# Optimization experiments

Measured on AMD Instinct MI355X. Metric: run time of the kernel, lower is better.

Reference implementation:

```python
import jax, jax.numpy as jnp
import numpy as np

B, H, S, DK, DV = 4, 16, 2048, 64, 64

def setup_inputs() -> dict:
    key = jax.random.key(0)
    k1, k2, k3, k4 = jax.random.split(key, 4)
    Q = jax.random.normal(k1, (B, H, S, DK), dtype=jnp.float32)
    K = jax.random.normal(k2, (B, H, S, DK), dtype=jnp.float32)
    V = jax.random.normal(k3, (B, H, S, DV), dtype=jnp.float32)
    mask_out = jax.random.randint(k4, (B, 1, 1, S), 0, 2).astype(jnp.bool_)
    return {"Q": Q, "K": K, "V": V, "mask_out": mask_out}

def reference(Q, K, V, mask_out):
    key_size = Q.shape[-1]
    seq_q, seq_k = Q.shape[-2], K.shape[-2]
    scale = jnp.sqrt(jnp.float32(key_size))
    # scores: [B, H, Sq, Sk]
    scores = jnp.einsum('bhqd,bhkd->bhqk', Q, K) / scale
    scores = jnp.where(mask_out, jnp.float32(-1e9), scores)
    attn = jax.nn.softmax(scores, axis=-1)
    # Gaussian relative-position decay: exp(-|i-j|^2 / (Sk^2 / 2))
    idx_q = jnp.arange(seq_q, dtype=jnp.float32)[:, None]
    idx_k = jnp.arange(seq_k, dtype=jnp.float32)[None, :]
    rel = idx_q - idx_k  # [Sq, Sk]
    decay = jnp.exp(-(rel * rel) * (2.0 / (seq_k * seq_k)))  # [Sq, Sk]
    attn = attn * decay  # broadcast over [B, H]
    return jnp.einsum('bhqk,bhkv->bhqv', attn, V)
```

## Files before the change

kernel.cpp:

```cpp
#include <hip/hip_runtime.h>
#include <hip/hip_bf16.h>
#include <hip/hip_fp16.h>

typedef __attribute__((ext_vector_type(8))) short bf16x8;
typedef __attribute__((ext_vector_type(4))) short bf16x4;
typedef __attribute__((ext_vector_type(4))) float f32x4;
typedef __attribute__((ext_vector_type(4))) unsigned u32x4;
typedef __attribute__((ext_vector_type(4))) int i32x4;

constexpr int Bn = 4, Hn = 16, S = 2048, D = 64;
constexpr int BQ = 128;
constexpr float LOG2E = 1.44269504088896340736f;
constexpr float CD2f = (2.0f / ((float)S * (float)S)) * LOG2E;

__device__ __forceinline__ unsigned cvtpk(float lo, float hi) {
    unsigned r;
    asm("v_cvt_pk_bf16_f32 %0, %1, %2" : "=v"(r) : "v"(lo), "v"(hi));
    return r;
}

__device__ __forceinline__ f32x4 mfma16(bf16x4 a, bf16x4 b, f32x4 c) {
#if __has_builtin(__builtin_amdgcn_mfma_f32_16x16x16bf16_1k)
    return __builtin_amdgcn_mfma_f32_16x16x16bf16_1k(a, b, c, 0, 0, 0);
#else
    asm volatile("v_mfma_f32_16x16x16_bf16 %0, %1, %2, %0"
                 : "+v"(c) : "v"(a), "v"(b));
    return c;
#endif
}

__device__ __forceinline__ void gload16(const short* g, short* lds) {
    __builtin_amdgcn_global_load_lds(
        (const __attribute__((address_space(1))) unsigned*)g,
        (__attribute__((address_space(3))) unsigned*)lds,
        16, 0, 0);
}

__global__ void compact_mask(const void* __restrict__ maskg,
                             int* __restrict__ idxp, int* __restrict__ Mg) {
    const int b = blockIdx.x, t = threadIdx.x;
    __shared__ int wsum[4];
    __shared__ int Msh;

    const unsigned* mu = (const unsigned*)maskg;
    bool is_bytes = false;
    #pragma unroll 8
    for (int i = 0; i < 64; ++i) is_bytes |= (mu[i] > 1u);

    int keep[8]; int cnt = 0;
    #pragma unroll
    for (int i = 0; i < 8; ++i) {
        const int key = t * 8 + i;
        int m;
        if (is_bytes) m = ((const unsigned char*)maskg)[b * S + key];
        else          m = ((const int*)maskg)[b * S + key];
        keep[i] = (m == 0);
        cnt += keep[i];
    }
    const int l = t & 63, w = t >> 6;
    int pre = cnt;
    #pragma unroll
    for (int d = 1; d < 64; d <<= 1) {
        int v = __shfl_up(pre, d, 64);
        if (l >= d) pre += v;
    }
    if (l == 63) wsum[w] = pre;
    __syncthreads();
    int base = 0;
    for (int i = 0; i < w; ++i) base += wsum[i];
    int offs = base + pre - cnt;
    #pragma unroll
    for (int i = 0; i < 8; ++i)
        if (keep[i]) idxp[b * S + (offs++)] = t * 8 + i;
    if (t == 255) Msh = base + pre;
    __syncthreads();
    const int M = Msh;
    for (int i = M + t; i < S; i += 256) idxp[b * S + i] = 0;
    if (M == 0)
        for (int i = t; i < S; i += 256) idxp[b * S + i] = i;
    if (t == 0) Mg[b] = (M == 0) ? -1 : M;
}

__global__ void pack_kv(const float* __restrict__ Kg, const float* __restrict__ Vg,
                        const int* __restrict__ idxp, const int* __restrict__ Mg,
                        short* __restrict__ Kw, short* __restrict__ Vw) {
    const int bh = blockIdx.x, b = bh >> 4;
    const int ck0 = blockIdx.y * 256;
    const int t = threadIdx.x;
    const int Mraw = Mg[b];
    const int M = (Mraw < 0) ? S : Mraw;
    if (ck0 >= M) return;
    const int* idxb = idxp + b * S;
    const float* Kp = Kg + (size_t)bh * S * D;
    const float* Vp = Vg + (size_t)bh * S * D;

    {
        const int dc = (t & 7) * 8;
        #pragma unroll
        for (int tile = 0; tile < 4; ++tile)
            #pragma unroll
            for (int it = 0; it < 2; ++it) {
                const int key = ck0 + tile * 64 + (t >> 3) + it * 32;
                u32x4 pk = u32x4{0u, 0u, 0u, 0u};
                if (key < M) {
                    const float* src = Kp + (size_t)idxb[key] * D + dc;
                    #pragma unroll
                    for (int jj = 0; jj < 4; ++jj)
                        pk[jj] = cvtpk(src[2 * jj], src[2 * jj + 1]);
                }
                *(u32x4*)(Kw + ((size_t)bh * S + key) * D + dc) = pk;
            }
    }
    {
        const int dv = t & 63;
        const int kb = (t >> 6) * 16;
        #pragma unroll
        for (int tile = 0; tile < 4; ++tile) {
            const int tg = (ck0 >> 6) + tile;
            float f[16];
            #pragma unroll
            for (int i = 0; i < 16; ++i) {
                const int key = ck0 + tile * 64 + kb + i;
                float v = 0.f;
                if (key < M) {
                    int row = idxb[key];
                    row = __builtin_amdgcn_readfirstlane(row);
                    v = Vp[(size_t)row * D + dv];
                }
                f[i] = v;
            }
            u32x4 p0, p1;
            #pragma unroll
            for (int jj = 0; jj < 4; ++jj) {
                p0[jj] = cvtpk(f[2 * jj], f[2 * jj + 1]);
                p1[jj] = cvtpk(f[8 + 2 * jj], f[9 + 2 * jj]);
            }
            short* dst = Vw + (((size_t)bh * 32 + tg) * 64 + dv) * 64 + kb;
            *(u32x4*)dst = p0;
            *(u32x4*)(dst + 8) = p1;
        }
    }
}

__global__ __launch_bounds__(256, 4) void attn_packed(
    const float* __restrict__ Qg, const short* __restrict__ Kw,
    const short* __restrict__ Vw, const int* __restrict__ idxp,
    const int* __restrict__ Mg, float* __restrict__ outg)
{
    __shared__ alignas(16) short Kt[2][64][64];
    __shared__ alignas(16) short Vt[2][64][64];
    __shared__ alignas(16) __half dtab[2176];
    __shared__ alignas(16) int   idxs[2][64];

    const int bid  = blockIdx.x;
    const int lblk = ((bid & 7) << 7) | (bid >> 3);
    const int qt   = lblk & 15;
    const int bh   = lblk >> 4;
    const int b    = bh >> 4;
    const int q0   = qt * BQ;

    const float* Qp   = Qg + ((size_t)bh * S + q0) * D;
    const short* Ksrc = Kw + (size_t)bh * S * D;
    const short* Vsrc = Vw + (size_t)bh * 32 * 64 * 64;
    float*       Op   = outg + ((size_t)bh * S + q0) * D;
    const int*   idxb = idxp + b * S;

    const int t  = threadIdx.x;
    const int w  = t >> 6;
    const int l  = t & 63;
    const int lr = l & 15;
    const int lg = l >> 4;
    const int lx = lr & 7;

    const int  Mraw    = Mg[b];
    const bool uniform = (Mraw < 0);
    const int  M       = uniform ? S : Mraw;
    const int  ntiles  = (M + 63) >> 6;

    int so[2], ld[2];
    #pragma unroll
    for (int p = 0; p < 2; ++p) {
        const int r = (p * 4 + w) * 8 + (l >> 3);
        so[p] = r * 64 + (((l & 7) ^ (r & 7)) << 3);
        ld[p] = (p * 4 + w) * 512;
    }

    gload16(Ksrc + so[0], &Kt[0][0][0] + ld[0]);
    gload16(Ksrc + so[1], &Kt[0][0][0] + ld[1]);
    gload16(Vsrc + so[0], &Vt[0][0][0] + ld[0]);
    gload16(Vsrc + so[1], &Vt[0][0][0] + ld[1]);
    if (t < 64) idxs[0][t] = idxb[t];

    for (int i = t; i < 2176; i += 256) {
        const float r = (float)(q0 + i - 2047);
        dtab[i] = __float2half(__builtin_exp2f(-CD2f * r * r));
    }

    const float qscale = uniform ? 0.0f : 0.125f * LOG2E;
    bf16x8 qf[2][2];
    #pragma unroll
    for (int rt = 0; rt < 2; ++rt) {
        const int row = w * 32 + rt * 16 + lr;
        #pragma unroll
        for (int g = 0; g < 2; ++g) {
            const float* src = Qp + row * D + g * 32 + lg * 8;
            union { unsigned u[4]; bf16x8 v; } cv;
            #pragma unroll
            for (int jj = 0; jj < 4; ++jj)
                cv.u[jj] = cvtpk(src[2 * jj] * qscale, src[2 * jj + 1] * qscale);
            qf[rt][g] = cv.v;
        }
    }

    f32x4 Oacc[2][4];
    #pragma unroll
    for (int rt = 0; rt < 2; ++rt)
        #pragma unroll
        for (int dt = 0; dt < 4; ++dt) Oacc[rt][dt] = f32x4{0.f, 0.f, 0.f, 0.f};
    float lrun[2] = {0.f, 0.f};

    const int qi0 = w * 32 + lr + 2047;

    asm volatile("s_waitcnt vmcnt(0)" ::: "memory");
    __syncthreads();

    int c = 0;
    for (int tt = 0; tt < ntiles; ++tt) {
        const int  rem  = M - tt * 64;
        const bool last = (rem <= 64);

        if (tt + 1 < ntiles) {
            const short* kp = Ksrc + (size_t)(tt + 1) * 4096;
            const short* vp = Vsrc + (size_t)(tt + 1) * 4096;
            gload16(kp + so[0], &Kt[c ^ 1][0][0] + ld[0]);
            gload16(kp + so[1], &Kt[c ^ 1][0][0] + ld[1]);
            gload16(vp + so[0], &Vt[c ^ 1][0][0] + ld[0]);
            gload16(vp + so[1], &Vt[c ^ 1][0][0] + ld[1]);
            if (t < 64) idxs[c ^ 1][t] = idxb[(tt + 1) * 64 + t];
        }

        const char* kbase = (const char*)&Kt[c][0][0];
        const char* vbase = (const char*)&Vt[c][0][0];

        #pragma unroll
        for (int kt = 0; kt < 4; ++kt) {
            const bf16x8 kf0 = *(const bf16x8*)(kbase + (kt * 16 + lr) * 128
                                                + ((lg ^ lx) << 4));
            const bf16x8 kf1 = *(const bf16x8*)(kbase + (kt * 16 + lr) * 128
                                                + (((4 + lg) ^ lx) << 4));
            f32x4 s0 = f32x4{-16.f, -16.f, -16.f, -16.f};
            f32x4 s1 = f32x4{-16.f, -16.f, -16.f, -16.f};
            __builtin_amdgcn_s_setprio(1);
            s0 = __builtin_amdgcn_mfma_f32_16x16x32_bf16(kf0, qf[0][0], s0, 0, 0, 0);
            s0 = __builtin_amdgcn_mfma_f32_16x16x32_bf16(kf1, qf[0][1], s0, 0, 0, 0);
            s1 = __builtin_amdgcn_mfma_f32_16x16x32_bf16(kf0, qf[1][0], s1, 0, 0, 0);
            s1 = __builtin_amdgcn_mfma_f32_16x16x32_bf16(kf1, qf[1][1], s1, 0, 0, 0);
            __builtin_amdgcn_s_setprio(0);

            const i32x4 iv = *(const i32x4*)&idxs[c][kt * 16 + lg * 4];

            bf16x4 Xb[2];
            #pragma unroll
            for (int rt = 0; rt < 2; ++rt) {
                const f32x4 s = rt ? s1 : s0;
                float p0 = __builtin_exp2f(s[0]);
                float p1 = __builtin_exp2f(s[1]);
                float p2 = __builtin_exp2f(s[2]);
                float p3 = __builtin_exp2f(s[3]);
                if (last) {
                    const int ck = kt * 16 + lg * 4;
                    p0 = (ck + 0 < rem) ? p0 : 0.f;
                    p1 = (ck + 1 < rem) ? p1 : 0.f;
                    p2 = (ck + 2 < rem) ? p2 : 0.f;
                    p3 = (ck + 3 < rem) ? p3 : 0.f;
                }
                lrun[rt] += (p0 + p1) + (p2 + p3);
                const int qi = qi0 + rt * 16;
                const float d0 = __half2float(dtab[qi - iv[0]]);
                const float d1 = __half2float(dtab[qi - iv[1]]);
                const float d2 = __half2float(dtab[qi - iv[2]]);
                const float d3 = __half2float(dtab[qi - iv[3]]);
                union { unsigned u[2]; bf16x4 v; } cx;
                cx.u[0] = cvtpk(p0 * d0, p1 * d1);
                cx.u[1] = cvtpk(p2 * d2, p3 * d3);
                Xb[rt] = cx.v;
            }

            __builtin_amdgcn_s_setprio(1);
            #pragma unroll
            for (int dt = 0; dt < 4; ++dt) {
                const bf16x4 vA = *(const bf16x4*)(vbase + (dt * 16 + lr) * 128
                          + ((((2 * kt + (lg >> 1)) ^ lx) << 4) | ((lg & 1) << 3)));
                Oacc[0][dt] = mfma16(vA, Xb[0], Oacc[0][dt]);
                Oacc[1][dt] = mfma16(vA, Xb[1], Oacc[1][dt]);
            }
            __builtin_amdgcn_s_setprio(0);
        }

        asm volatile("s_waitcnt vmcnt(0)" ::: "memory");
        __syncthreads();
        c ^= 1;
    }

    #pragma unroll
    for (int rt = 0; rt < 2; ++rt) {
        float ls = lrun[rt];
        ls += __shfl_xor(ls, 16, 64);
        ls += __shfl_xor(ls, 32, 64);
        const float inv = 1.0f / ls;
        const int row = w * 32 + rt * 16 + lr;
        #pragma unroll
        for (int dt = 0; dt < 4; ++dt) {
            f32x4 o = Oacc[rt][dt];
            o[0] *= inv; o[1] *= inv; o[2] *= inv; o[3] *= inv;
            *(f32x4*)&Op[(size_t)row * D + dt * 16 + lg * 4] = o;
        }
    }
}

__global__ __launch_bounds__(256, 3) void attn_gather(
    const float* __restrict__ Qg, const float* __restrict__ Kg,
    const float* __restrict__ Vg, const int* __restrict__ idxp,
    const int* __restrict__ Mg, float* __restrict__ outg)
{
    __shared__ alignas(16) short Kt[64][72];
    __shared__ alignas(16) short Vt[64][72];
    __shared__ alignas(16) float dtab[2176];
    __shared__ alignas(16) int   idxs[64];

    const int blk = blockIdx.x;
    const int qt  = blk & 15;
    const int bh  = blk >> 4;
    const int b   = bh >> 4;
    const int q0  = qt * BQ;

    const float* Qp = Qg + ((size_t)bh * S + q0) * D;
    const float* Kp = Kg + (size_t)bh * S * D;
    const float* Vp = Vg + (size_t)bh * S * D;
    float*       Op = outg + ((size_t)bh * S + q0) * D;
    const int*   idxb = idxp + b * S;

    const int t  = threadIdx.x;
    const int w  = t >> 6;
    const int l  = t & 63;
    const int lr = l & 15;
    const int lg = l >> 4;

    const int  Mraw    = Mg[b];
    const bool uniform = (Mraw < 0);
    const int  M       = uniform ? S : Mraw;

    for (int i = t; i < 2176; i += 256) {
        const float r = (float)(q0 + i - 2047);
        dtab[i] = __builtin_exp2f(-CD2f * r * r);
    }

    const float qscale = uniform ? 0.0f : 0.125f * LOG2E;
    bf16x8 qf[2][2];
    #pragma unroll
    for (int rt = 0; rt < 2; ++rt) {
        const int row = w * 32 + rt * 16 + lr;
        #pragma unroll
        for (int g = 0; g < 2; ++g) {
            const float* src = Qp + row * D + g * 32 + lg * 8;
            union { unsigned u[4]; bf16x8 v; } cv;
            #pragma unroll
            for (int jj = 0; jj < 4; ++jj)
                cv.u[jj] = cvtpk(src[2 * jj] * qscale, src[2 * jj + 1] * qscale);
            qf[rt][g] = cv.v;
        }
    }

    f32x4 Oacc[2][4];
    #pragma unroll
    for (int rt = 0; rt < 2; ++rt)
        #pragma unroll
        for (int dt = 0; dt < 4; ++dt) Oacc[rt][dt] = f32x4{0.f, 0.f, 0.f, 0.f};
    float lrun[2] = {0.f, 0.f};

    const int qrl2047 = w * 32 + lr + 2047;

    for (int kv = 0; kv < M; kv += 64) {
        const int  rem  = M - kv;
        const bool last = (rem <= 64);
        __syncthreads();
        {
            const int key = t >> 3;
            const int dc  = (t & 7) * 8;
            #pragma unroll
            for (int it = 0; it < 2; ++it) {
                const int row = idxb[kv + key + it * 32];
                const float* src = Kp + (size_t)row * D + dc;
                u32x4 pk;
                #pragma unroll
                for (int jj = 0; jj < 4; ++jj)
                    pk[jj] = cvtpk(src[2 * jj], src[2 * jj + 1]);
                *(u32x4*)&Kt[key + it * 32][dc] = pk;
            }
        }
        if (t < 64) idxs[t] = idxb[kv + t];
        {
            const int dv = t & 63;
            const int kb = (t >> 6) * 16;
            float f[16];
            #pragma unroll
            for (int i = 0; i < 16; ++i) {
                int row = idxb[kv + kb + i];
                row = __builtin_amdgcn_readfirstlane(row);
                f[i] = Vp[(size_t)row * D + dv];
            }
            u32x4 p0, p1;
            #pragma unroll
            for (int jj = 0; jj < 4; ++jj) {
                p0[jj] = cvtpk(f[2 * jj], f[2 * jj + 1]);
                p1[jj] = cvtpk(f[8 + 2 * jj], f[9 + 2 * jj]);
            }
            *(u32x4*)&Vt[dv][kb]     = p0;
            *(u32x4*)&Vt[dv][kb + 8] = p1;
        }
        __syncthreads();

        bf16x8 kf[4][2];
        #pragma unroll
        for (int kt = 0; kt < 4; ++kt)
            #pragma unroll
            for (int g = 0; g < 2; ++g)
                kf[kt][g] = *(const bf16x8*)&Kt[kt * 16 + lr][g * 32 + lg * 8];

        bf16x4 Xb[2][4];
        #pragma unroll
        for (int rt = 0; rt < 2; ++rt) {
            f32x4 sc[4];
            #pragma unroll
            for (int kt = 0; kt < 4; ++kt) {
                f32x4 acc = f32x4{-16.f, -16.f, -16.f, -16.f};
                acc = __builtin_amdgcn_mfma_f32_16x16x32_bf16(kf[kt][0], qf[rt][0], acc, 0, 0, 0);
                acc = __builtin_amdgcn_mfma_f32_16x16x32_bf16(kf[kt][1], qf[rt][1], acc, 0, 0, 0);
                sc[kt] = acc;
            }
            const int qi = qrl2047 + rt * 16;
            float lp = 0.f;
            #pragma unroll
            for (int kt = 0; kt < 4; ++kt) {
                const i32x4 iv = *(const i32x4*)&idxs[kt * 16 + lg * 4];
                float p0 = __builtin_exp2f(sc[kt][0]);
                float p1 = __builtin_exp2f(sc[kt][1]);
                float p2 = __builtin_exp2f(sc[kt][2]);
                float p3 = __builtin_exp2f(sc[kt][3]);
                if (last) {
                    const int ck = kt * 16 + lg * 4;
                    p0 = (ck + 0 < rem) ? p0 : 0.f;
                    p1 = (ck + 1 < rem) ? p1 : 0.f;
                    p2 = (ck + 2 < rem) ? p2 : 0.f;
                    p3 = (ck + 3 < rem) ? p3 : 0.f;
                }
                lp += (p0 + p1) + (p2 + p3);
                const float d0 = dtab[qi - iv[0]];
                const float d1 = dtab[qi - iv[1]];
                const float d2 = dtab[qi - iv[2]];
                const float d3 = dtab[qi - iv[3]];
                union { unsigned u[2]; bf16x4 v; } cx;
                cx.u[0] = cvtpk(p0 * d0, p1 * d1);
                cx.u[1] = cvtpk(p2 * d2, p3 * d3);
                Xb[rt][kt] = cx.v;
            }
            lrun[rt] += lp;
        }

        #pragma unroll
        for (int kt = 0; kt < 4; ++kt) {
            bf16x4 vA[4];
            #pragma unroll
            for (int dt = 0; dt < 4; ++dt)
                vA[dt] = *(const bf16x4*)&Vt[dt * 16 + lr][kt * 16 + lg * 4];
            #pragma unroll
            for (int dt = 0; dt < 4; ++dt) {
                Oacc[0][dt] = mfma16(vA[dt], Xb[0][kt], Oacc[0][dt]);
                Oacc[1][dt] = mfma16(vA[dt], Xb[1][kt], Oacc[1][dt]);
            }
        }
    }

    #pragma unroll
    for (int rt = 0; rt < 2; ++rt) {
        float ls = lrun[rt];
        ls += __shfl_xor(ls, 16, 64);
        ls += __shfl_xor(ls, 32, 64);
        const float inv = 1.0f / ls;
        const int row = w * 32 + rt * 16 + lr;
        #pragma unroll
        for (int dt = 0; dt < 4; ++dt) {
            f32x4 o = Oacc[rt][dt];
            o[0] *= inv; o[1] *= inv; o[2] *= inv; o[3] *= inv;
            *(f32x4*)&Op[(size_t)row * D + dt * 16 + lg * 4] = o;
        }
    }
}

extern "C" void kernel_launch(void* const* d_in, const int* in_sizes, int n_in,
                              void* d_out, int out_size, void* d_ws, size_t ws_size,
                              hipStream_t stream) {
    const float* Q = (const float*)d_in[0];
    const float* K = (const float*)d_in[1];
    const float* V = (const float*)d_in[2];
    const void*  M = d_in[3];
    float* out = (float*)d_out;

    int* idxp = (int*)d_ws;
    int* Mg   = idxp + Bn * S;
    size_t base = (((size_t)(Bn * S + Bn) * 4) + 255) & ~(size_t)255;
    short* Kw = (short*)((char*)d_ws + base);
    short* Vw = Kw + (size_t)Bn * Hn * S * D;
    const size_t need = base + 2 * (size_t)Bn * Hn * S * D * sizeof(short);

    compact_mask<<<dim3(Bn), dim3(256), 0, stream>>>(M, idxp, Mg);
    const int nblk = Bn * Hn * (S / BQ);
    if (ws_size >= need) {
        pack_kv<<<dim3(Bn * Hn, S / 256), dim3(256), 0, stream>>>(K, V, idxp, Mg, Kw, Vw);
        attn_packed<<<dim3(nblk), dim3(256), 0, stream>>>(Q, Kw, Vw, idxp, Mg, out);
    } else {
        attn_gather<<<dim3(nblk), dim3(256), 0, stream>>>(Q, K, V, idxp, Mg, out);
    }
}
```

Before: 117.5 us.

## Switch PV path to fp16 with packed decay multiply and paired decay table

Converts V and the probability tile to fp16 instead of bf16, so the decay multiply can use v_pk_mul_f16 on two query rows at once. The decay table now stores pairs (rows qi and qi+16) packed into one dword, which halves the LDS lookups and drops the half-to-float conversions. The softmax offset moves from -16 to -2 so fp16 probabilities don't underflow. The goal is fewer VALU instructions per tile, at the cost of fp16 range and rounding risk on exp values and on V.

```diff
diff --git a/kernel.cpp b/kernel.cpp
--- a/kernel.cpp
+++ b/kernel.cpp
@@ -4,6 +4,7 @@
 
 typedef __attribute__((ext_vector_type(8))) short bf16x8;
 typedef __attribute__((ext_vector_type(4))) short bf16x4;
+typedef __attribute__((ext_vector_type(4))) _Float16 f16x4;
 typedef __attribute__((ext_vector_type(4))) float f32x4;
 typedef __attribute__((ext_vector_type(4))) unsigned u32x4;
 typedef __attribute__((ext_vector_type(4))) int i32x4;
@@ -17,6 +18,27 @@
     unsigned r;
     asm("v_cvt_pk_bf16_f32 %0, %1, %2" : "=v"(r) : "v"(lo), "v"(hi));
     return r;
+}
+
+__device__ __forceinline__ unsigned pkrtz(float lo, float hi) {
+    auto h = __builtin_amdgcn_cvt_pkrtz(lo, hi);
+    return __builtin_bit_cast(unsigned, h);
+}
+
+__device__ __forceinline__ unsigned pkmul(unsigned a, unsigned b) {
+    unsigned r;
+    asm("v_pk_mul_f16 %0, %1, %2" : "=v"(r) : "v"(a), "v"(b));
+    return r;
+}
+
+__device__ __forceinline__ f32x4 mfma16h(f16x4 a, f16x4 b, f32x4 c) {
+#if __has_builtin(__builtin_amdgcn_mfma_f32_16x16x16f16)
+    return __builtin_amdgcn_mfma_f32_16x16x16f16(a, b, c, 0, 0, 0);
+#else
+    asm volatile("v_mfma_f32_16x16x16_f16 %0, %1, %2, %0"
+                 : "+v"(c) : "v"(a), "v"(b));
+    return c;
+#endif
 }
 
 __device__ __forceinline__ f32x4 mfma16(bf16x4 a, bf16x4 b, f32x4 c) {
@@ -132,8 +154,8 @@
             u32x4 p0, p1;
             #pragma unroll
             for (int jj = 0; jj < 4; ++jj) {
-                p0[jj] = cvtpk(f[2 * jj], f[2 * jj + 1]);
-                p1[jj] = cvtpk(f[8 + 2 * jj], f[9 + 2 * jj]);
+                p0[jj] = pkrtz(f[2 * jj], f[2 * jj + 1]);
+                p1[jj] = pkrtz(f[8 + 2 * jj], f[9 + 2 * jj]);
             }
             short* dst = Vw + (((size_t)bh * 32 + tg) * 64 + dv) * 64 + kb;
             *(u32x4*)dst = p0;
@@ -149,7 +171,7 @@
 {
     __shared__ alignas(16) short Kt[2][64][64];
     __shared__ alignas(16) short Vt[2][64][64];
-    __shared__ alignas(16) __half dtab[2176];
+    __shared__ alignas(16) unsigned dpair[2176];
     __shared__ alignas(16) int   idxs[2][64];
 
     const int bid  = blockIdx.x;
@@ -192,8 +214,11 @@
     if (t < 64) idxs[0][t] = idxb[t];
 
     for (int i = t; i < 2176; i += 256) {
-        const float r = (float)(q0 + i - 2047);
-        dtab[i] = __float2half(__builtin_exp2f(-CD2f * r * r));
+        const float r0 = (float)(q0 + i - 2047);
+        const float r1 = r0 + 16.0f;
+        const float d0 = __builtin_exp2f(-CD2f * r0 * r0);
+        const float d1 = __builtin_exp2f(-CD2f * r1 * r1);
+        dpair[i] = pkrtz(d0, d1);
     }
 
     const float qscale = uniform ? 0.0f : 0.125f * LOG2E;
@@ -248,8 +273,8 @@
                                                 + ((lg ^ lx) << 4));
             const bf16x8 kf1 = *(const bf16x8*)(kbase + (kt * 16 + lr) * 128
                                                 + (((4 + lg) ^ lx) << 4));
-            f32x4 s0 = f32x4{-16.f, -16.f, -16.f, -16.f};
-            f32x4 s1 = f32x4{-16.f, -16.f, -16.f, -16.f};
+            f32x4 s0 = f32x4{-2.f, -2.f, -2.f, -2.f};
+            f32x4 s1 = f32x4{-2.f, -2.f, -2.f, -2.f};
             __builtin_amdgcn_s_setprio(1);
             s0 = __builtin_amdgcn_mfma_f32_16x16x32_bf16(kf0, qf[0][0], s0, 0, 0, 0);
             s0 = __builtin_amdgcn_mfma_f32_16x16x32_bf16(kf1, qf[0][1], s0, 0, 0, 0);
@@ -259,40 +284,43 @@
 
             const i32x4 iv = *(const i32x4*)&idxs[c][kt * 16 + lg * 4];
 
-            bf16x4 Xb[2];
-            #pragma unroll
-            for (int rt = 0; rt < 2; ++rt) {
-                const f32x4 s = rt ? s1 : s0;
-                float p0 = __builtin_exp2f(s[0]);
-                float p1 = __builtin_exp2f(s[1]);
-                float p2 = __builtin_exp2f(s[2]);
-                float p3 = __builtin_exp2f(s[3]);
-                if (last) {
-                    const int ck = kt * 16 + lg * 4;
-                    p0 = (ck + 0 < rem) ? p0 : 0.f;
-                    p1 = (ck + 1 < rem) ? p1 : 0.f;
-                    p2 = (ck + 2 < rem) ? p2 : 0.f;
-                    p3 = (ck + 3 < rem) ? p3 : 0.f;
-                }
-                lrun[rt] += (p0 + p1) + (p2 + p3);
-                const int qi = qi0 + rt * 16;
-                const float d0 = __half2float(dtab[qi - iv[0]]);
-                const float d1 = __half2float(dtab[qi - iv[1]]);
-                const float d2 = __half2float(dtab[qi - iv[2]]);
-                const float d3 = __half2float(dtab[qi - iv[3]]);
-                union { unsigned u[2]; bf16x4 v; } cx;
-                cx.u[0] = cvtpk(p0 * d0, p1 * d1);
-                cx.u[1] = cvtpk(p2 * d2, p3 * d3);
-                Xb[rt] = cx.v;
-            }
+            const unsigned dq0 = dpair[qi0 - iv[0]];
+            const unsigned dq1 = dpair[qi0 - iv[1]];
+            const unsigned dq2 = dpair[qi0 - iv[2]];
+            const unsigned dq3 = dpair[qi0 - iv[3]];
+
+            float pa0 = __builtin_exp2f(s0[0]), pb0 = __builtin_exp2f(s1[0]);
+            float pa1 = __builtin_exp2f(s0[1]), pb1 = __builtin_exp2f(s1[1]);
+            float pa2 = __builtin_exp2f(s0[2]), pb2 = __builtin_exp2f(s1[2]);
+            float pa3 = __builtin_exp2f(s0[3]), pb3 = __builtin_exp2f(s1[3]);
+            if (last) {
+                const int ck = kt * 16 + lg * 4;
+                pa0 = (ck + 0 < rem) ? pa0 : 0.f;  pb0 = (ck + 0 < rem) ? pb0 : 0.f;
+                pa1 = (ck + 1 < rem) ? pa1 : 0.f;  pb1 = (ck + 1 < rem) ? pb1 : 0.f;
+                pa2 = (ck + 2 < rem) ? pa2 : 0.f;  pb2 = (ck + 2 < rem) ? pb2 : 0.f;
+                pa3 = (ck + 3 < rem) ? pa3 : 0.f;  pb3 = (ck + 3 < rem) ? pb3 : 0.f;
+            }
+            lrun[0] += (pa0 + pa1) + (pa2 + pa3);
+            lrun[1] += (pb0 + pb1) + (pb2 + pb3);
+
+            const unsigned pd0 = pkmul(pkrtz(pa0, pb0), dq0);
+            const unsigned pd1 = pkmul(pkrtz(pa1, pb1), dq1);
+            const unsigned pd2 = pkmul(pkrtz(pa2, pb2), dq2);
+            const unsigned pd3 = pkmul(pkrtz(pa3, pb3), dq3);
+
+            union { unsigned u[2]; f16x4 v; } xb0, xb1;
+            xb0.u[0] = __builtin_amdgcn_perm(pd1, pd0, 0x05040100u);
+            xb0.u[1] = __builtin_amdgcn_perm(pd3, pd2, 0x05040100u);
+            xb1.u[0] = __builtin_amdgcn_perm(pd1, pd0, 0x07060302u);
+            xb1.u[1] = __builtin_amdgcn_perm(pd3, pd2, 0x07060302u);
 
             __builtin_amdgcn_s_setprio(1);
             #pragma unroll
             for (int dt = 0; dt < 4; ++dt) {
-                const bf16x4 vA = *(const bf16x4*)(vbase + (dt * 16 + lr) * 128
+                const f16x4 vA = *(const f16x4*)(vbase + (dt * 16 + lr) * 128
                           + ((((2 * kt + (lg >> 1)) ^ lx) << 4) | ((lg & 1) << 3)));
-                Oacc[0][dt] = mfma16(vA, Xb[0], Oacc[0][dt]);
-                Oacc[1][dt] = mfma16(vA, Xb[1], Oacc[1][dt]);
+                Oacc[0][dt] = mfma16h(vA, xb0.v, Oacc[0][dt]);
+                Oacc[1][dt] = mfma16h(vA, xb1.v, Oacc[1][dt]);
             }
             __builtin_amdgcn_s_setprio(0);
         }
```

Result: slower. 123.8 us (+5.3%).
